# Performance work log

Measured on AMD Instinct MI355X. Metric: run time of the kernel, lower is better.

## Reference

```python
import jax, jax.numpy as jnp
import numpy as np

DEG2RAD = np.pi / 180.0
EARTH_RADIUS_KM = 6371.009


def setup_inputs() -> dict:
    key = jax.random.key(0)
    ks = jax.random.split(key, 7)
    B = 8388608
    return {
        "pred_": jax.random.normal(ks[0], (B, 2), dtype=jnp.float32),
        "true_": jax.random.normal(ks[1], (B, 2), dtype=jnp.float32),
        "mean_speed": jax.random.normal(ks[2], (2,), dtype=jnp.float32),
        "std_speed": jax.random.uniform(ks[3], (2,), dtype=jnp.float32, minval=0.5, maxval=1.5),
        "site": jax.random.normal(ks[4], (B, 2), dtype=jnp.float32) * 30.0,
        "mean": jax.random.normal(ks[5], (2,), dtype=jnp.float32),
        "std": jax.random.uniform(ks[6], (2,), dtype=jnp.float32, minval=0.5, maxval=1.5),
    }


def reference(pred_, true_, mean_speed, std_speed, site, mean, std):
    # Denormalize site coords and speed deltas, then offset by site (broadcast over last dim of size 2).
    site_d = site * std + mean                       # [B,2]
    pred = pred_ * std_speed + mean_speed + site_d   # [B,2] absolute (lat, lng)
    true = true_ * std_speed + mean_speed + site_d   # [B,2]

    # _range(): clamp only the predicted latitude to [-90, 90].
    lat1 = jnp.clip(pred[:, 0], -90.0, 90.0) * DEG2RAD
    lng1 = pred[:, 1] * DEG2RAD
    lat2 = true[:, 0] * DEG2RAD
    lng2 = true[:, 1] * DEG2RAD

    sin_lat1, cos_lat1 = jnp.sin(lat1), jnp.cos(lat1)
    sin_lat2, cos_lat2 = jnp.sin(lat2), jnp.cos(lat2)
    delta = lng2 - lng1
    cos_d, sin_d = jnp.cos(delta), jnp.sin(delta)

    # Great-circle central angle via atan2 (Vincenty special case for a sphere).
    num = jnp.sqrt((cos_lat2 * sin_d) ** 2 + (cos_lat1 * sin_lat2 - sin_lat1 * cos_lat2 * cos_d) ** 2)
    den = sin_lat1 * sin_lat2 + cos_lat1 * cos_lat2 * cos_d
    gd = EARTH_RADIUS_KM * jnp.arctan2(num, den)     # [B] distances in km

    b = pred_.shape[0]
    return (jnp.sum(gd) / b)[None]                   # shape (1,), matching torch sum_gd / b
```

## Files before the change

kernel.cpp:

```cpp
#include <hip/hip_runtime.h>
#include <math.h>

#define DEG2RAD 0.017453292519943295f
#define EARTH_R 6371.009f
#define NBLOCKS 4096

__device__ __forceinline__ float gd_one(float plat, float plng, float tlat, float tlng) {
    float lat1 = fminf(fmaxf(plat, -90.0f), 90.0f) * DEG2RAD;
    float lng1 = plng * DEG2RAD;
    float lat2 = tlat * DEG2RAD;
    float lng2 = tlng * DEG2RAD;

    float s1 = __sinf(lat1), c1 = __cosf(lat1);
    float s2 = __sinf(lat2), c2 = __cosf(lat2);
    float d  = lng2 - lng1;
    float cd = __cosf(d),  sd = __sinf(d);

    float t0 = c2 * sd;
    float t1 = c1 * s2 - s1 * c2 * cd;
    float num = sqrtf(t0 * t0 + t1 * t1);
    float den = s1 * s2 + c1 * c2 * cd;
    return EARTH_R * atan2f(num, den);
}

__global__ __launch_bounds__(256) void gd_main(
    const float4* __restrict__ pred,
    const float4* __restrict__ tru,
    const float4* __restrict__ site,
    const float*  __restrict__ mean_speed,
    const float*  __restrict__ std_speed,
    const float*  __restrict__ mean,
    const float*  __restrict__ stdv,
    float*        __restrict__ partials,
    int n4)
{
    const float ms0 = mean_speed[0], ms1 = mean_speed[1];
    const float ss0 = std_speed[0],  ss1 = std_speed[1];
    const float m0  = mean[0],       m1  = mean[1];
    const float s0  = stdv[0],       s1  = stdv[1];

    float local = 0.0f;
    const int stride = gridDim.x * blockDim.x;
    for (int i = blockIdx.x * blockDim.x + threadIdx.x; i < n4; i += stride) {
        float4 p  = pred[i];
        float4 t  = tru[i];
        float4 st = site[i];

        float sdlat_a = st.x * s0 + m0;
        float sdlng_a = st.y * s1 + m1;
        float sdlat_b = st.z * s0 + m0;
        float sdlng_b = st.w * s1 + m1;

        local += gd_one(p.x * ss0 + ms0 + sdlat_a, p.y * ss1 + ms1 + sdlng_a,
                        t.x * ss0 + ms0 + sdlat_a, t.y * ss1 + ms1 + sdlng_a);
        local += gd_one(p.z * ss0 + ms0 + sdlat_b, p.w * ss1 + ms1 + sdlng_b,
                        t.z * ss0 + ms0 + sdlat_b, t.w * ss1 + ms1 + sdlng_b);
    }

    #pragma unroll
    for (int off = 32; off > 0; off >>= 1)
        local += __shfl_down(local, off, 64);

    __shared__ float wsum[4];
    const int lane = threadIdx.x & 63;
    const int wid  = threadIdx.x >> 6;
    if (lane == 0) wsum[wid] = local;
    __syncthreads();
    if (threadIdx.x == 0)
        partials[blockIdx.x] = wsum[0] + wsum[1] + wsum[2] + wsum[3];
}

__global__ __launch_bounds__(256) void gd_final(
    const float* __restrict__ partials, int n,
    float* __restrict__ out, double invB)
{
    double local = 0.0;
    for (int i = threadIdx.x; i < n; i += 256)
        local += (double)partials[i];

    #pragma unroll
    for (int off = 32; off > 0; off >>= 1)
        local += __shfl_down(local, off, 64);

    __shared__ double wsum[4];
    const int lane = threadIdx.x & 63;
    const int wid  = threadIdx.x >> 6;
    if (lane == 0) wsum[wid] = local;
    __syncthreads();
    if (threadIdx.x == 0)
        out[0] = (float)((wsum[0] + wsum[1] + wsum[2] + wsum[3]) * invB);
}

extern "C" void kernel_launch(void* const* d_in, const int* in_sizes, int n_in,
                              void* d_out, int out_size, void* d_ws, size_t ws_size,
                              hipStream_t stream) {
    const float4* pred = (const float4*)d_in[0];
    const float4* tru  = (const float4*)d_in[1];
    const float*  msp  = (const float*)d_in[2];
    const float*  ssp  = (const float*)d_in[3];
    const float4* site = (const float4*)d_in[4];
    const float*  mn   = (const float*)d_in[5];
    const float*  sd   = (const float*)d_in[6];

    const int total = in_sizes[0];
    const int n4    = total / 4;
    const long long B = total / 2;

    float* partials = (float*)d_ws;

    gd_main<<<NBLOCKS, 256, 0, stream>>>(pred, tru, site, msp, ssp, mn, sd, partials, n4);
    gd_final<<<1, 256, 0, stream>>>(partials, NBLOCKS, (float*)d_out, 1.0 / (double)B);
}
```

Measured before the change: 208.3 us.

## Use polynomial atan2, fixed per-block chunking with front-loaded loads, hoisted radius scale

Replaces the libm atan2f with a minimax polynomial atan2 built on a hardware reciprocal, specialised for a non-negative numerator, and uses the raw hardware sqrt. The grid-stride loop becomes a fixed grid where each thread issues all twelve float4 loads up front, giving more memory parallelism. The Earth-radius multiply moves into the final scale. This cuts transcendental ALU cost and latency but assumes the size divides by 1024 and slightly changes accuracy.

```diff
diff --git a/kernel.cpp b/kernel.cpp
--- a/kernel.cpp
+++ b/kernel.cpp
@@ -2,8 +2,22 @@
 #include <math.h>
 
 #define DEG2RAD 0.017453292519943295f
-#define EARTH_R 6371.009f
-#define NBLOCKS 4096
+#define EARTH_R 6371.009
+#define PI_F    3.14159265358979f
+#define PIO2_F  1.57079632679490f
+
+__device__ __forceinline__ float atan2_pos(float num, float den) {
+    float ad = __builtin_fabsf(den);
+    float mn = fminf(num, ad);
+    float mx = fmaxf(num, ad);
+    float t  = mn * __builtin_amdgcn_rcpf(mx);
+    float u  = t * t;
+    float a  = t * (0.99997726f + u * (-0.33262347f + u * (0.19354346f +
+               u * (-0.11643287f + u * (0.05265332f + u * (-0.01172120f))))));
+    a = (num > ad)   ? (PIO2_F - a) : a;
+    a = (den < 0.0f) ? (PI_F  - a) : a;
+    return a;
+}
 
 __device__ __forceinline__ float gd_one(float plat, float plng, float tlat, float tlng) {
     float lat1 = fminf(fmaxf(plat, -90.0f), 90.0f) * DEG2RAD;
@@ -18,12 +32,12 @@
 
     float t0 = c2 * sd;
     float t1 = c1 * s2 - s1 * c2 * cd;
-    float num = sqrtf(t0 * t0 + t1 * t1);
+    float num = __builtin_amdgcn_sqrtf(t0 * t0 + t1 * t1);
     float den = s1 * s2 + c1 * c2 * cd;
-    return EARTH_R * atan2f(num, den);
+    return atan2_pos(num, den);
 }
 
-__global__ __launch_bounds__(256) void gd_main(
+__global__ __launch_bounds__(256, 6) void gd_main(
     const float4* __restrict__ pred,
     const float4* __restrict__ tru,
     const float4* __restrict__ site,
@@ -31,31 +45,34 @@
     const float*  __restrict__ std_speed,
     const float*  __restrict__ mean,
     const float*  __restrict__ stdv,
-    float*        __restrict__ partials,
-    int n4)
+    float*        __restrict__ partials)
 {
     const float ms0 = mean_speed[0], ms1 = mean_speed[1];
     const float ss0 = std_speed[0],  ss1 = std_speed[1];
     const float m0  = mean[0],       m1  = mean[1];
     const float s0  = stdv[0],       s1  = stdv[1];
 
+    const int base = blockIdx.x * 1024 + threadIdx.x;
+
+    float4 p0 = pred[base], p1 = pred[base + 256], p2 = pred[base + 512], p3 = pred[base + 768];
+    float4 t0 = tru [base], t1 = tru [base + 256], t2 = tru [base + 512], t3 = tru [base + 768];
+    float4 q0 = site[base], q1 = site[base + 256], q2 = site[base + 512], q3 = site[base + 768];
+
     float local = 0.0f;
-    const int stride = gridDim.x * blockDim.x;
-    for (int i = blockIdx.x * blockDim.x + threadIdx.x; i < n4; i += stride) {
-        float4 p  = pred[i];
-        float4 t  = tru[i];
-        float4 st = site[i];
-
-        float sdlat_a = st.x * s0 + m0;
-        float sdlng_a = st.y * s1 + m1;
-        float sdlat_b = st.z * s0 + m0;
-        float sdlng_b = st.w * s1 + m1;
-
-        local += gd_one(p.x * ss0 + ms0 + sdlat_a, p.y * ss1 + ms1 + sdlng_a,
-                        t.x * ss0 + ms0 + sdlat_a, t.y * ss1 + ms1 + sdlng_a);
-        local += gd_one(p.z * ss0 + ms0 + sdlat_b, p.w * ss1 + ms1 + sdlng_b,
-                        t.z * ss0 + ms0 + sdlat_b, t.w * ss1 + ms1 + sdlng_b);
+    #define DO_PAIR(P, T, Q)                                                         \
+    {                                                                                \
+        float sa = (Q).x * s0 + m0, sb = (Q).y * s1 + m1;                            \
+        float sc = (Q).z * s0 + m0, sd_ = (Q).w * s1 + m1;                           \
+        local += gd_one((P).x * ss0 + ms0 + sa,  (P).y * ss1 + ms1 + sb,             \
+                        (T).x * ss0 + ms0 + sa,  (T).y * ss1 + ms1 + sb);            \
+        local += gd_one((P).z * ss0 + ms0 + sc,  (P).w * ss1 + ms1 + sd_,            \
+                        (T).z * ss0 + ms0 + sc,  (T).w * ss1 + ms1 + sd_);           \
     }
+    DO_PAIR(p0, t0, q0)
+    DO_PAIR(p1, t1, q1)
+    DO_PAIR(p2, t2, q2)
+    DO_PAIR(p3, t3, q3)
+    #undef DO_PAIR
 
     #pragma unroll
     for (int off = 32; off > 0; off >>= 1)
@@ -72,7 +89,7 @@
 
 __global__ __launch_bounds__(256) void gd_final(
     const float* __restrict__ partials, int n,
-    float* __restrict__ out, double invB)
+    float* __restrict__ out, double scale)
 {
     double local = 0.0;
     for (int i = threadIdx.x; i < n; i += 256)
@@ -88,7 +105,7 @@
     if (lane == 0) wsum[wid] = local;
     __syncthreads();
     if (threadIdx.x == 0)
-        out[0] = (float)((wsum[0] + wsum[1] + wsum[2] + wsum[3]) * invB);
+        out[0] = (float)((wsum[0] + wsum[1] + wsum[2] + wsum[3]) * scale);
 }
 
 extern "C" void kernel_launch(void* const* d_in, const int* in_sizes, int n_in,
@@ -105,9 +122,11 @@
     const int total = in_sizes[0];
     const int n4    = total / 4;
     const long long B = total / 2;
+    const int blocks = n4 / 1024;
 
     float* partials = (float*)d_ws;
 
-    gd_main<<<NBLOCKS, 256, 0, stream>>>(pred, tru, site, msp, ssp, mn, sd, partials, n4);
-    gd_final<<<1, 256, 0, stream>>>(partials, NBLOCKS, (float*)d_out, 1.0 / (double)B);
+    gd_main<<<blocks, 256, 0, stream>>>(pred, tru, site, msp, ssp, mn, sd, partials);
+    gd_final<<<1, 256, 0, stream>>>(partials, blocks, (float*)d_out,
+                                    EARTH_R / (double)B);
 }
```

Result: no change. 207.2 us (-0.6%).
